# Kernel tuning notes

Hardware: AMD Instinct MI355X
Metric: run time of the kernel (lower is better)

Reference implementation:

```python
import jax, jax.numpy as jnp
import numpy as np

B, W, D = 8, 1024, 1024
HEADS, KDIM, VDIM = 16, 64, 64


def setup_inputs() -> dict:
    key = jax.random.key(0)
    k1, k2, k3, k4 = jax.random.split(key, 4)
    # he_normal-ish scaling for weights
    s = (2.0 / D) ** 0.5
    return {
        "inputs": jax.random.normal(k1, (B, W, D), dtype=jnp.float32),
        "Wq": jax.random.normal(k2, (D, HEADS * KDIM), dtype=jnp.float32) * s,
        "Wk": jax.random.normal(k3, (D, HEADS * KDIM), dtype=jnp.float32) * s,
        "Wv": jax.random.normal(k4, (D, HEADS * VDIM), dtype=jnp.float32) * s,
    }


def reference(inputs, Wq, Wk, Wv):
    # Self-attention: memory = inputs
    bsz, win, _ = inputs.shape
    # DenseHeads: linear projection, reshaped to (B, W, heads, head_units)
    q = (inputs @ Wq).reshape(bsz, win, HEADS, KDIM)
    k = (inputs @ Wk).reshape(bsz, win, HEADS, KDIM)
    v = (inputs @ Wv).reshape(bsz, win, HEADS, VDIM)
    scale = KDIM ** (-0.5)
    # scores[b,q,h,m] = sum_k Q[b,q,h,k] * K[b,m,h,k]
    scores = jnp.einsum("bqhk,bmhk->bqhm", q, k) * scale
    attn = jax.nn.softmax(scores, axis=-1)
    # out[b,q,h,v] = sum_m attn[b,q,h,m] * V[b,m,h,v]
    out = jnp.einsum("bqhm,bmhv->bqhv", attn, v)
    return out
```

## Files before the change

### kernel.cpp

```cpp
#include <hip/hip_runtime.h>
#include <stdint.h>


using bf16x8 = __attribute__((ext_vector_type(8))) __bf16;
using f32x4  = __attribute__((ext_vector_type(4))) float;
using f16x4  = __attribute__((ext_vector_type(4))) _Float16;

union frag_u  { uint4 u4; bf16x8 f; };
union vfrag_u { uint2 u2; f16x4 f; };
union pfrag_u { unsigned int u[2]; f16x4 f; };

__device__ inline unsigned short f2bf(float x){
  unsigned int u = __float_as_uint(x);
  u += 0x7fffu + ((u >> 16) & 1u);
  return (unsigned short)(u >> 16);
}

__device__ inline unsigned int pkrtz_u32(float a, float b){
  auto r = __builtin_amdgcn_cvt_pkrtz(a, b);
  unsigned int u; __builtin_memcpy(&u, &r, 4); return u;
}

__device__ inline void gl_lds16(const void* g, void* l){
  __builtin_amdgcn_global_load_lds(
      (const __attribute__((address_space(1))) void*)g,
      (__attribute__((address_space(3))) void*)l, 16, 0, 0);
}

#define SBAR() do{ asm volatile("" ::: "memory"); __builtin_amdgcn_s_barrier(); asm volatile("" ::: "memory"); }while(0)
#define VMC(n)  asm volatile("s_waitcnt vmcnt(" #n ")" ::: "memory")

__global__ void cast_all(const float* __restrict__ X,
                         const float* __restrict__ Wq, const float* __restrict__ Wk,
                         const float* __restrict__ Wv,
                         unsigned short* __restrict__ Xb,
                         unsigned short* __restrict__ Wt){
  __shared__ float tile[64][65];
  int bid = blockIdx.x;
  if (bid < 8192){
    int i = (bid * 256 + threadIdx.x) * 4;
    float4 v = *(const float4*)(X + i);
    ushort4 o;
    o.x = f2bf(v.x); o.y = f2bf(v.y); o.z = f2bf(v.z); o.w = f2bf(v.w);
    *(ushort4*)(Xb + i) = o;
    return;
  }
  int id = bid - 8192;
  int proj = id >> 8;
  int rem  = id & 255;
  int kt = rem & 15, nt = rem >> 4;
  const float* Wsrc = (proj == 0) ? Wq : ((proj == 1) ? Wk : Wv);
  int k0 = kt * 64, n0 = nt * 64;
  int tx = threadIdx.x & 63, ty = threadIdx.x >> 6;
  for (int i = 0; i < 16; i++){
    int k = i * 4 + ty;
    tile[k][tx] = Wsrc[(k0 + k) * 1024 + n0 + tx];
  }
  __syncthreads();
  for (int i = 0; i < 16; i++){
    int n = i * 4 + ty;
    Wt[(proj * 1024 + n0 + n) * 1024 + k0 + tx] = f2bf(tile[tx][n]);
  }
}

__global__ __launch_bounds__(1024, 4) void gemm_qkv(
    const unsigned short* __restrict__ Xb,
    const unsigned short* __restrict__ Wt,
    unsigned short* __restrict__ QK,
    unsigned short* __restrict__ Vt){
  __shared__ __align__(16) char Abuf[2][32768];
  __shared__ __align__(16) char Bbuf[2][24576];

  int bid = blockIdx.x;
  int tau = (bid & 7) * 64 + (bid >> 3);
  int by = tau >> 4, bx = tau & 15;
  int tid = threadIdx.x;
  int w = tid >> 6, lane = tid & 63;
  int li = lane & 15, g = lane >> 4;
  int lrow = lane >> 3;
  int wr = w >> 2, wc = w & 3;
  int wu = __builtin_amdgcn_readfirstlane(w);

  int xcol = ((lane & 7) ^ lrow) << 3;
  int aoff0 = (by * 256 + w * 8 + lrow) * 1024 + xcol;
  int aoff1 = (by * 256 + (16 + w) * 8 + lrow) * 1024 + xcol;
  int bseg0 = (w < 8) ? w : (w + 8);
  int bseg1 = w + 8;
  int boff0 = (bx * 192 + bseg0 * 8 + lrow) * 1024 + xcol;
  int boff1 = (bx * 192 + bseg1 * 8 + lrow) * 1024 + xcol;

  int swz  = (li & 7) << 4;
  int colA0 = (g * 16) ^ swz;
  int colA1 = (64 + g * 16) ^ swz;
  int aBase = (wr * 64 + li) * 128;
  int bBase = (wc * 48 + li) * 128;

  f32x4 acc[4][3] = {};
  frag_u bfr[3][2], af[2][2];

#define LDB(buf) do{ \
  _Pragma("unroll") for (int n = 0; n < 3; n++){ \
    bfr[n][0].u4 = *(const uint4*)&Bbuf[buf][bBase + n * 2048 + colA0]; \
    bfr[n][1].u4 = *(const uint4*)&Bbuf[buf][bBase + n * 2048 + colA1]; } }while(0)
#define LDA2(buf, m0) do{ \
  af[0][0].u4 = *(const uint4*)&Abuf[buf][aBase + (m0)     * 2048 + colA0]; \
  af[0][1].u4 = *(const uint4*)&Abuf[buf][aBase + (m0)     * 2048 + colA1]; \
  af[1][0].u4 = *(const uint4*)&Abuf[buf][aBase + (m0 + 1) * 2048 + colA0]; \
  af[1][1].u4 = *(const uint4*)&Abuf[buf][aBase + (m0 + 1) * 2048 + colA1]; }while(0)
#define MFMA6(P) do{ __builtin_amdgcn_s_setprio(1); \
  _Pragma("unroll") for (int kk = 0; kk < 2; kk++) \
  _Pragma("unroll") for (int i = 0; i < 2; i++) \
  _Pragma("unroll") for (int n = 0; n < 3; n++) \
    acc[(P) + i][n] = __builtin_amdgcn_mfma_f32_16x16x32_bf16( \
        af[i][kk].f, bfr[n][kk].f, acc[(P) + i][n], 0, 0, 0); \
  __builtin_amdgcn_s_setprio(0); }while(0)

  gl_lds16(Wt + boff0, &Bbuf[0][bseg0 * 1024]);
  if (wu < 8) gl_lds16(Wt + boff1, &Bbuf[0][bseg1 * 1024]);
  gl_lds16(Xb + aoff0, &Abuf[0][w * 1024]);
  gl_lds16(Xb + aoff1, &Abuf[0][(16 + w) * 1024]);
  gl_lds16(Wt + boff0 + 64, &Bbuf[1][bseg0 * 1024]);
  if (wu < 8){
    gl_lds16(Wt + boff1 + 64, &Bbuf[1][bseg1 * 1024]);
    VMC(2);
  } else {
    VMC(1);
  }
  SBAR();

  for (int t = 0; t < 16; ++t){
    int cur = t & 1, nxt = cur ^ 1;
    LDB(cur);
    LDA2(cur, 0);
    if (t < 15){
      gl_lds16(Xb + aoff0 + (t + 1) * 64, &Abuf[nxt][w * 1024]);
      gl_lds16(Xb + aoff1 + (t + 1) * 64, &Abuf[nxt][(16 + w) * 1024]);
    }
    MFMA6(0);
    SBAR();
    LDA2(cur, 2);
    if (t < 14){
      gl_lds16(Wt + boff0 + (t + 2) * 64, &Bbuf[cur][bseg0 * 1024]);
      if (wu < 8) gl_lds16(Wt + boff1 + (t + 2) * 64, &Bbuf[cur][bseg1 * 1024]);
    }
    MFMA6(2);
    if (t < 14){
      if (wu < 8) { VMC(2); } else { VMC(1); }
    } else if (t == 14) {
      VMC(0);
    }
    SBAR();
  }
#undef LDB
#undef LDA2
#undef MFMA6

  int row0 = by * 256 + wr * 64 + g * 4;
  int bb16 = (by >> 2) * 16;
#pragma unroll
  for (int n = 0; n < 3; n++){
    int cb = bx * 192 + wc * 48 + n * 16;
    if (cb < 2048){
      float sc = (cb < 1024) ? 0.1803368801111f : 1.0f;
#pragma unroll
      for (int m = 0; m < 4; m++){
        int row = row0 + m * 16;
#pragma unroll
        for (int r = 0; r < 4; r++)
          QK[(size_t)(row + r) * 2048 + cb + li] = f2bf(acc[m][n][r] * sc);
      }
    } else {
      int vc = cb + li - 2048;
      int hh = vc >> 6, dd = vc & 63;
#pragma unroll
      for (int m = 0; m < 4; m++){
        int mtok = (row0 + m * 16) & 1023;
        uint2 cv;
        cv.x = pkrtz_u32(acc[m][n][0], acc[m][n][1]);
        cv.y = pkrtz_u32(acc[m][n][2], acc[m][n][3]);
        *(uint2*)(Vt + ((size_t)(bb16 + hh) * 64 + dd) * 1024 + mtok) = cv;
      }
    }
  }
}

__global__ __launch_bounds__(256, 4) void attn(const unsigned short* __restrict__ QK,
                                               const unsigned short* __restrict__ Vt,
                                               float* __restrict__ Out){
  __shared__ __align__(16) unsigned short Kbuf[64 * 64];
  __shared__ __align__(16) unsigned short Vbuf[64 * 64];
  int id = blockIdx.x;
  int bh = id & 127, qb = id >> 7;
  int b = bh >> 4, h = bh & 15;
  int w = threadIdx.x >> 6, lane = threadIdx.x & 63;
  int g = lane >> 4, li = lane & 15;
  int lrow = lane >> 3, lcol = lane & 7;
  int scol = ((lcol ^ lrow) & 7) * 8;

  frag_u qf[2];
  {
    int tok = b * 1024 + qb * 64 + w * 16 + li;
    const unsigned short* qp = QK + (size_t)tok * 2048 + h * 64 + g * 8;
    qf[0].u4 = *(const uint4*)(qp);
    qf[1].u4 = *(const uint4*)(qp + 32);
  }

  f32x4 o[4] = {};
  f32x4 osum = {};
  const f32x4 bias = {-10.f, -10.f, -10.f, -10.f};
  pfrag_u ones;
  ones.u[0] = 0x3c003c00u; ones.u[1] = 0x3c003c00u;

  const unsigned short* Kg = QK + (size_t)b * 1024 * 2048 + 1024 + h * 64;
  const unsigned short* Vg = Vt + (size_t)bh * 65536;

  for (int mt = 0; mt < 16; mt++){
    int m0 = mt * 64;
    __syncthreads();
    for (int i = 0; i < 2; i++){
      int idx = w * 2 + i;
      int row = idx * 8 + lrow;
      gl_lds16(Kg + (size_t)(m0 + row) * 2048 + scol, Kbuf + idx * 512);
      gl_lds16(Vg + row * 1024 + m0 + scol,           Vbuf + idx * 512);
    }
    __syncthreads();

    f32x4 s[4];
    for (int t = 0; t < 4; t++) s[t] = bias;
    for (int t = 0; t < 4; t++){
      for (int c = 0; c < 2; c++){
        frag_u kf;
        kf.u4 = *(const uint4*)(Kbuf + (t * 16 + li) * 64 + ((((c << 2) + g) ^ (li & 7)) << 3));
        s[t] = __builtin_amdgcn_mfma_f32_16x16x32_bf16(kf.f, qf[c].f, s[t], 0, 0, 0);
      }
    }

    pfrag_u pf[4];
    for (int t = 0; t < 4; t++){
      float p0 = __builtin_exp2f(s[t][0]);
      float p1 = __builtin_exp2f(s[t][1]);
      float p2 = __builtin_exp2f(s[t][2]);
      float p3 = __builtin_exp2f(s[t][3]);
      pf[t].u[0] = pkrtz_u32(p0, p1);
      pf[t].u[1] = pkrtz_u32(p2, p3);
    }

    for (int t = 0; t < 4; t++)
      osum = __builtin_amdgcn_mfma_f32_16x16x16f16(ones.f, pf[t].f, osum, 0, 0, 0);
    for (int tv = 0; tv < 4; tv++){
      for (int t = 0; t < 4; t++){
        int gg = ((t * 2 + (g >> 1)) ^ (li & 7));
        vfrag_u vf;
        vf.u2 = *(const uint2*)(Vbuf + (tv * 16 + li) * 64 + gg * 8 + (g & 1) * 4);
        o[tv] = __builtin_amdgcn_mfma_f32_16x16x16f16(vf.f, pf[t].f, o[tv], 0, 0, 0);
      }
    }
  }

  float inv = 1.f / osum[0];

  int tok = b * 1024 + qb * 64 + w * 16 + li;
  float* op = Out + (size_t)tok * 1024 + h * 64 + g * 4;
  for (int tv = 0; tv < 4; tv++){
    float4 v4;
    v4.x = o[tv][0] * inv; v4.y = o[tv][1] * inv;
    v4.z = o[tv][2] * inv; v4.w = o[tv][3] * inv;
    *(float4*)(op + tv * 16) = v4;
  }
}

extern "C" void kernel_launch(void* const* d_in, const int* in_sizes, int n_in,
                              void* d_out, int out_size, void* d_ws, size_t ws_size,
                              hipStream_t stream) {
  const float* X  = (const float*)d_in[0];
  const float* Wq = (const float*)d_in[1];
  const float* Wk = (const float*)d_in[2];
  const float* Wv = (const float*)d_in[3];
  float* Out = (float*)d_out;
  char* ws = (char*)d_ws;
  unsigned short* Xb = (unsigned short*)(ws);
  unsigned short* Wt = (unsigned short*)(ws + (size_t)16 * 1024 * 1024);
  unsigned short* QK = (unsigned short*)(ws + (size_t)22 * 1024 * 1024);
  unsigned short* Vt = (unsigned short*)(ws + (size_t)54 * 1024 * 1024);

  cast_all<<<8960, 256, 0, stream>>>(X, Wq, Wk, Wv, Xb, Wt);
  gemm_qkv<<<512, 1024, 0, stream>>>(Xb, Wt, QK, Vt);
  attn    <<<2048, 256, 0, stream>>>(QK, Vt, Out);
}
```

Measured before the change: 208.1 us.

## Tune cast, attention softmax sum, exp intrinsic, and occupancy across kernels

```diff
diff --git a/kernel.cpp b/kernel.cpp
--- a/kernel.cpp
+++ b/kernel.cpp
@@ -19,6 +19,14 @@
 __device__ inline unsigned int pkrtz_u32(float a, float b){
   auto r = __builtin_amdgcn_cvt_pkrtz(a, b);
   unsigned int u; __builtin_memcpy(&u, &r, 4); return u;
+}
+
+__device__ inline float fexp2(float x){
+#if __has_builtin(__builtin_amdgcn_exp2f)
+  return __builtin_amdgcn_exp2f(x);
+#else
+  float r; asm("v_exp_f32 %0, %1\n\ts_nop 0" : "=v"(r) : "v"(x)); return r;
+#endif
 }
 
 __device__ inline void gl_lds16(const void* g, void* l){
@@ -37,15 +45,18 @@
                          unsigned short* __restrict__ Wt){
   __shared__ float tile[64][65];
   int bid = blockIdx.x;
-  if (bid < 8192){
-    int i = (bid * 256 + threadIdx.x) * 4;
-    float4 v = *(const float4*)(X + i);
-    ushort4 o;
-    o.x = f2bf(v.x); o.y = f2bf(v.y); o.z = f2bf(v.z); o.w = f2bf(v.w);
-    *(ushort4*)(Xb + i) = o;
+  if (bid < 2048){
+#pragma unroll
+    for (int it = 0; it < 4; it++){
+      int i = ((bid * 4 + it) * 256 + threadIdx.x) * 4;
+      float4 v = *(const float4*)(X + i);
+      ushort4 o;
+      o.x = f2bf(v.x); o.y = f2bf(v.y); o.z = f2bf(v.z); o.w = f2bf(v.w);
+      *(ushort4*)(Xb + i) = o;
+    }
     return;
   }
-  int id = bid - 8192;
+  int id = bid - 2048;
   int proj = id >> 8;
   int rem  = id & 255;
   int kt = rem & 15, nt = rem >> 4;
@@ -107,13 +118,12 @@
   af[0][1].u4 = *(const uint4*)&Abuf[buf][aBase + (m0)     * 2048 + colA1]; \
   af[1][0].u4 = *(const uint4*)&Abuf[buf][aBase + (m0 + 1) * 2048 + colA0]; \
   af[1][1].u4 = *(const uint4*)&Abuf[buf][aBase + (m0 + 1) * 2048 + colA1]; }while(0)
-#define MFMA6(P) do{ __builtin_amdgcn_s_setprio(1); \
+#define MFMA6(P) do{ \
   _Pragma("unroll") for (int kk = 0; kk < 2; kk++) \
   _Pragma("unroll") for (int i = 0; i < 2; i++) \
   _Pragma("unroll") for (int n = 0; n < 3; n++) \
     acc[(P) + i][n] = __builtin_amdgcn_mfma_f32_16x16x32_bf16( \
-        af[i][kk].f, bfr[n][kk].f, acc[(P) + i][n], 0, 0, 0); \
-  __builtin_amdgcn_s_setprio(0); }while(0)
+        af[i][kk].f, bfr[n][kk].f, acc[(P) + i][n], 0, 0, 0); }while(0)
 
   gl_lds16(Wt + boff0, &Bbuf[0][bseg0 * 1024]);
   if (wu < 8) gl_lds16(Wt + boff1, &Bbuf[0][bseg1 * 1024]);
@@ -184,7 +194,7 @@
   }
 }
 
-__global__ __launch_bounds__(256, 4) void attn(const unsigned short* __restrict__ QK,
+__global__ __launch_bounds__(256, 8) void attn(const unsigned short* __restrict__ QK,
                                                const unsigned short* __restrict__ Vt,
                                                float* __restrict__ Out){
   __shared__ __align__(16) unsigned short Kbuf[64 * 64];
@@ -206,10 +216,8 @@
   }
 
   f32x4 o[4] = {};
-  f32x4 osum = {};
+  float psum = 0.f;
   const f32x4 bias = {-10.f, -10.f, -10.f, -10.f};
-  pfrag_u ones;
-  ones.u[0] = 0x3c003c00u; ones.u[1] = 0x3c003c00u;
 
   const unsigned short* Kg = QK + (size_t)b * 1024 * 2048 + 1024 + h * 64;
   const unsigned short* Vg = Vt + (size_t)bh * 65536;
@@ -226,8 +234,11 @@
     __syncthreads();
 
     f32x4 s[4];
+#pragma unroll
     for (int t = 0; t < 4; t++) s[t] = bias;
+#pragma unroll
     for (int t = 0; t < 4; t++){
+#pragma unroll
       for (int c = 0; c < 2; c++){
         frag_u kf;
         kf.u4 = *(const uint4*)(Kbuf + (t * 16 + li) * 64 + ((((c << 2) + g) ^ (li & 7)) << 3));
@@ -236,18 +247,20 @@
     }
 
     pfrag_u pf[4];
+#pragma unroll
     for (int t = 0; t < 4; t++){
-      float p0 = __builtin_exp2f(s[t][0]);
-      float p1 = __builtin_exp2f(s[t][1]);
-      float p2 = __builtin_exp2f(s[t][2]);
-      float p3 = __builtin_exp2f(s[t][3]);
+      float p0 = fexp2(s[t][0]);
+      float p1 = fexp2(s[t][1]);
+      float p2 = fexp2(s[t][2]);
+      float p3 = fexp2(s[t][3]);
+      psum += (p0 + p1) + (p2 + p3);
       pf[t].u[0] = pkrtz_u32(p0, p1);
       pf[t].u[1] = pkrtz_u32(p2, p3);
     }
 
-    for (int t = 0; t < 4; t++)
-      osum = __builtin_amdgcn_mfma_f32_16x16x16f16(ones.f, pf[t].f, osum, 0, 0, 0);
+#pragma unroll
     for (int tv = 0; tv < 4; tv++){
+#pragma unroll
       for (int t = 0; t < 4; t++){
         int gg = ((t * 2 + (g >> 1)) ^ (li & 7));
         vfrag_u vf;
@@ -257,10 +270,13 @@
     }
   }
 
-  float inv = 1.f / osum[0];
-
+  float tot = psum;
+  tot += __shfl_xor(tot, 16);
+  tot += __shfl_xor(tot, 32);
+  float inv = 1.f / tot;
   int tok = b * 1024 + qb * 64 + w * 16 + li;
   float* op = Out + (size_t)tok * 1024 + h * 64 + g * 4;
+#pragma unroll
   for (int tv = 0; tv < 4; tv++){
     float4 v4;
     v4.x = o[tv][0] * inv; v4.y = o[tv][1] * inv;
@@ -283,7 +299,7 @@
   unsigned short* QK = (unsigned short*)(ws + (size_t)22 * 1024 * 1024);
   unsigned short* Vt = (unsigned short*)(ws + (size_t)54 * 1024 * 1024);
 
-  cast_all<<<8960, 256, 0, stream>>>(X, Wq, Wk, Wv, Xb, Wt);
+  cast_all<<<2816, 256, 0, stream>>>(X, Wq, Wk, Wv, Xb, Wt);
   gemm_qkv<<<512, 1024, 0, stream>>>(Xb, Wt, QK, Vt);
   attn    <<<2048, 256, 0, stream>>>(QK, Vt, Out);
 }
```

Measured after the change: 228.8 us. +10.0%, slower.
